# Optimization experiments

Hardware: AMD Instinct MI355X
Metric: run time of the kernel (lower is better)

## Reference

```python
import jax, jax.numpy as jnp
import numpy as np

N_NODES = 100000


def gcn_conv(x, edge_index, W, b):
    # PyG GCNConv: linear first, then symmetric-normalized aggregation with self-loops, then bias.
    n = x.shape[0]
    h = x @ W  # [N, out]
    loop = jnp.arange(n, dtype=edge_index.dtype)
    src = jnp.concatenate([edge_index[0], loop])  # source nodes (x_j)
    dst = jnp.concatenate([edge_index[1], loop])  # target nodes (aggregation index)
    ones = jnp.ones(dst.shape[0], dtype=h.dtype)
    deg = jax.ops.segment_sum(ones, dst, num_segments=n)  # in-degree incl. self-loop
    dinv = jnp.where(deg > 0, jax.lax.rsqrt(deg), 0.0)
    norm = dinv[src] * dinv[dst]  # [E+N]
    msgs = h[src] * norm[:, None]  # gather + scale
    out = jax.ops.segment_sum(msgs, dst, num_segments=n)  # scatter-add
    return out + b


def setup_inputs() -> dict:
    key = jax.random.key(0)
    k1, k2, k3, k4 = jax.random.split(key, 4)
    x = jax.random.normal(k1, (N_NODES, 128), dtype=jnp.float32)
    edge_index = jax.random.randint(k2, (2, 3200000), 0, N_NODES, dtype=jnp.int64)
    W1 = jax.random.normal(k3, (128, 16), dtype=jnp.float32) * (1.0 / np.sqrt(128))
    b1 = jnp.zeros((16,), dtype=jnp.float32)
    W2 = jax.random.normal(k4, (16, 10), dtype=jnp.float32) * (1.0 / np.sqrt(16))
    b2 = jnp.zeros((10,), dtype=jnp.float32)
    return {"x": x, "edge_index": edge_index, "W1": W1, "b1": b1, "W2": W2, "b2": b2}


def reference(x, edge_index, W1, b1, W2, b2):
    h = gcn_conv(x, edge_index, W1, b1)
    h = jax.nn.relu(h)
    h = gcn_conv(h, edge_index, W2, b2)
    return jax.nn.log_softmax(h, axis=1)
```

## Files before the change

### kernel.cpp

```cpp
#include <hip/hip_runtime.h>
#include <hip/hip_fp16.h>
#include <math.h>

#define NN 100000
#define F0 128
#define F1 16
#define F2 10
#define NBUCK 391
#define TILE 8192
#define EPT 16
#define CAP 16384
#define BPT 512

__device__ inline void fma4(float4& a, float s, const float4& w) {
  a.x = fmaf(s, w.x, a.x);
  a.y = fmaf(s, w.y, a.y);
  a.z = fmaf(s, w.z, a.z);
  a.w = fmaf(s, w.w, a.w);
}

__device__ inline unsigned pk2(float a, float b) {
  __half ha = __float2half(a), hb = __float2half(b);
  return (unsigned)__half_as_ushort(ha) | ((unsigned)__half_as_ushort(hb) << 16);
}

__device__ inline float2 up2(unsigned u) {
  __half2 h;
  *(unsigned*)&h = u;
  return __half22float2(h);
}

__device__ inline void nt_store_f2(float a, float b, float* p) {
  union { double d; float f[2]; } u;
  u.f[0] = a; u.f[1] = b;
  __builtin_nontemporal_store(u.d, (double*)p);
}

__global__ void k_zero(int* __restrict__ bucket_cnt) {
  int i = blockIdx.x * blockDim.x + threadIdx.x;
  if (i < NBUCK) bucket_cnt[i] = 0;
}

__global__ __launch_bounds__(256) void k_bincount(const int* __restrict__ dst, int E,
                                                  int* __restrict__ bucket_cnt) {
  __shared__ int hist[NBUCK];
  int t = threadIdx.x;
  for (int i = t; i < NBUCK; i += 256) hist[i] = 0;
  __syncthreads();
  int per = (E + gridDim.x - 1) / gridDim.x;
  int e0 = blockIdx.x * per, e1 = min(E, e0 + per);
  for (int e = e0 + t; e < e1; e += 256)
    atomicAdd(&hist[__builtin_nontemporal_load(dst + e) >> 8], 1);
  __syncthreads();
  for (int i = t; i < NBUCK; i += 256)
    if (hist[i]) atomicAdd(&bucket_cnt[i], hist[i]);
}

__global__ void k_binscan(const int* __restrict__ bucket_cnt, int* __restrict__ bucket_base,
                          int* __restrict__ bucket_cur) {
  __shared__ int lds[512];
  int t = threadIdx.x;
  int v = (t < NBUCK) ? bucket_cnt[t] : 0;
  lds[t] = v;
  __syncthreads();
  for (int o = 1; o < 512; o <<= 1) {
    int add = (t >= o) ? lds[t - o] : 0;
    __syncthreads();
    lds[t] += add;
    __syncthreads();
  }
  if (t < NBUCK) {
    int excl = lds[t] - v;
    bucket_base[t] = excl;
    bucket_cur[t] = excl;
    if (t == NBUCK - 1) bucket_base[NBUCK] = lds[t];
  }
}

__global__ __launch_bounds__(BPT) void k_binplace(const int* __restrict__ src,
                                                  const int* __restrict__ dst, int E,
                                                  int* __restrict__ bucket_cur,
                                                  int* __restrict__ packed) {
  __shared__ int cnt[NBUCK];
  __shared__ int loff[NBUCK];
  __shared__ int gbase[NBUCK];
  __shared__ int part[256];
  __shared__ int stage[TILE];
  int t = threadIdx.x;
  int e0 = blockIdx.x * TILE, e1 = min(E, e0 + TILE);
  int total = e1 - e0;
  for (int i = t; i < NBUCK; i += BPT) cnt[i] = 0;
  __syncthreads();
  int bkpos[EPT];
  int pval[EPT];
#pragma unroll
  for (int k = 0; k < EPT; k++) {
    int e = e0 + t + k * BPT;
    if (e < e1) {
      int d = __builtin_nontemporal_load(dst + e);
      int s = __builtin_nontemporal_load(src + e);
      int bk = d >> 8;
      int pos = atomicAdd(&cnt[bk], 1);
      bkpos[k] = (bk << 13) | pos;
      pval[k] = (s << 8) | (d & 255);
    } else {
      bkpos[k] = -1;
    }
  }
  __syncthreads();
  for (int i = t; i < NBUCK; i += BPT) {
    int c = cnt[i];
    gbase[i] = c ? atomicAdd(&bucket_cur[i], c) : 0;
  }
  if (t < 256) {
    int i0 = 2 * t, i1 = 2 * t + 1;
    int c0 = (i0 < NBUCK) ? cnt[i0] : 0;
    int c1 = (i1 < NBUCK) ? cnt[i1] : 0;
    part[t] = c0 + c1;
  }
  __syncthreads();
  for (int o = 1; o < 256; o <<= 1) {
    int add = 0;
    if (t < 256 && t >= o) add = part[t - o];
    __syncthreads();
    if (t < 256) part[t] += add;
    __syncthreads();
  }
  if (t < 256) {
    int i0 = 2 * t, i1 = 2 * t + 1;
    int c0 = (i0 < NBUCK) ? cnt[i0] : 0;
    int c1 = (i1 < NBUCK) ? cnt[i1] : 0;
    int excl = part[t] - c0 - c1;
    if (i0 < NBUCK) loff[i0] = excl;
    if (i1 < NBUCK) loff[i1] = excl + c0;
  }
  __syncthreads();
#pragma unroll
  for (int k = 0; k < EPT; k++) {
    if (bkpos[k] >= 0) {
      int bk = bkpos[k] >> 13, pos = bkpos[k] & 8191;
      stage[loff[bk] + pos] = pval[k];
    }
  }
  __syncthreads();
  int sub = t >> 4, lane = t & 15;
  for (int bk = sub; bk < NBUCK; bk += BPT / 16) {
    int lo = loff[bk];
    int hi = (bk + 1 < NBUCK) ? loff[bk + 1] : total;
    int gb = gbase[bk];
    for (int i = lo + lane; i < hi; i += 16) packed[gb + (i - lo)] = stage[i];
  }
}

__global__ __launch_bounds__(256) void k_bucket(const int* __restrict__ packed,
                                                const int* __restrict__ bucket_base,
                                                int* __restrict__ row_start,
                                                float* __restrict__ dinv,
                                                int* __restrict__ col, int E) {
  __shared__ int stage[CAP];
  __shared__ int hist[256];
  __shared__ int off[256];
  __shared__ int cur[256];
  int b = blockIdx.x, t = threadIdx.x;
  int base = bucket_base[b];
  int cnt = bucket_base[b + 1] - base;
  hist[t] = 0;
  bool staged = (cnt <= CAP);
  if (staged)
    for (int i = t; i < cnt; i += 256) stage[i] = __builtin_nontemporal_load(packed + base + i);
  __syncthreads();
  if (staged) {
    for (int i = t; i < cnt; i += 256) atomicAdd(&hist[stage[i] & 255], 1);
  } else {
    for (int i = t; i < cnt; i += 256) atomicAdd(&hist[packed[base + i] & 255], 1);
  }
  __syncthreads();
  int v = hist[t];
  off[t] = v;
  __syncthreads();
  for (int o = 1; o < 256; o <<= 1) {
    int add = (t >= o) ? off[t - o] : 0;
    __syncthreads();
    off[t] += add;
    __syncthreads();
  }
  int excl = off[t] - v;
  cur[t] = excl;
  int d = b * 256 + t;
  if (d < NN) {
    row_start[d] = base + excl;
    dinv[d] = rsqrtf((float)(v + 1));
  }
  if (b == 0 && t == 0) row_start[NN] = E;
  __syncthreads();
  if (staged) {
    for (int i = t; i < cnt; i += 256) {
      int p = stage[i];
      int pos = atomicAdd(&cur[p & 255], 1);
      col[base + pos] = p >> 8;
    }
  } else {
    for (int i = t; i < cnt; i += 256) {
      int p = packed[base + i];
      int pos = atomicAdd(&cur[p & 255], 1);
      col[base + pos] = p >> 8;
    }
  }
}

__global__ __launch_bounds__(256) void k_lin1(const float* __restrict__ x,
                                              const float* __restrict__ W1,
                                              const float* __restrict__ dinv,
                                              unsigned* __restrict__ tab1) {
  __shared__ float4 wl[F0 * 4];
  int t = threadIdx.x;
  for (int i = t; i < F0 * 4; i += 256) wl[i] = ((const float4*)W1)[i];
  __syncthreads();
  int row0 = (blockIdx.x * 256 + t) * 4;
  if (row0 >= NN) return;
  float4 acc[4][4];
#pragma unroll
  for (int r = 0; r < 4; r++)
#pragma unroll
    for (int j = 0; j < 4; j++) acc[r][j] = make_float4(0.f, 0.f, 0.f, 0.f);
  const float4* xr0 = (const float4*)(x + (size_t)(row0 + 0) * F0);
  const float4* xr1 = (const float4*)(x + (size_t)(row0 + 1) * F0);
  const float4* xr2 = (const float4*)(x + (size_t)(row0 + 2) * F0);
  const float4* xr3 = (const float4*)(x + (size_t)(row0 + 3) * F0);
  for (int k4 = 0; k4 < F0 / 4; k4++) {
    float4 xv[4];
    xv[0] = xr0[k4]; xv[1] = xr1[k4]; xv[2] = xr2[k4]; xv[3] = xr3[k4];
#pragma unroll
    for (int kk = 0; kk < 4; kk++) {
      float4 w0 = wl[(k4 * 4 + kk) * 4 + 0];
      float4 w1 = wl[(k4 * 4 + kk) * 4 + 1];
      float4 w2 = wl[(k4 * 4 + kk) * 4 + 2];
      float4 w3 = wl[(k4 * 4 + kk) * 4 + 3];
#pragma unroll
      for (int r = 0; r < 4; r++) {
        float xs = kk == 0 ? xv[r].x : kk == 1 ? xv[r].y : kk == 2 ? xv[r].z : xv[r].w;
        fma4(acc[r][0], xs, w0);
        fma4(acc[r][1], xs, w1);
        fma4(acc[r][2], xs, w2);
        fma4(acc[r][3], xs, w3);
      }
    }
  }
#pragma unroll
  for (int r = 0; r < 4; r++) {
    float dd = dinv[row0 + r];
    float4 a0 = acc[r][0], a1 = acc[r][1], a2 = acc[r][2], a3 = acc[r][3];
    uint4 o0, o1;
    o0.x = pk2(dd * a0.x, dd * a0.y);
    o0.y = pk2(dd * a0.z, dd * a0.w);
    o0.z = pk2(dd * a1.x, dd * a1.y);
    o0.w = pk2(dd * a1.z, dd * a1.w);
    o1.x = pk2(dd * a2.x, dd * a2.y);
    o1.y = pk2(dd * a2.z, dd * a2.w);
    o1.z = pk2(dd * a3.x, dd * a3.y);
    o1.w = pk2(dd * a3.z, dd * a3.w);
    uint4* orow = (uint4*)(tab1 + (size_t)(row0 + r) * 8);
    orow[0] = o0;
    orow[1] = o1;
  }
}

__global__ __launch_bounds__(256) void k_agg1(const uint4* __restrict__ tab1,
                                              const int* __restrict__ row_start,
                                              const int* __restrict__ col,
                                              const float* __restrict__ dinv,
                                              const float* __restrict__ b1,
                                              const float* __restrict__ W2g,
                                              unsigned* __restrict__ tab2) {
  __shared__ float w2[F1][F2];
  __shared__ float b1l[F1];
  int t = threadIdx.x;
  if (t < F1 * F2) w2[t / F2][t % F2] = W2g[t];
  if (t < F1) b1l[t] = b1[t];
  __syncthreads();
  int g = blockIdx.x * 256 + t;
  int d = g >> 2, q = g & 3;
  if (d >= NN) return;
  float a[16];
#pragma unroll
  for (int j = 0; j < 16; j++) a[j] = 0.f;
  auto addrow = [&](int s) {
    uint4 v0 = tab1[2 * s];
    uint4 v1 = tab1[2 * s + 1];
    float2 f;
    f = up2(v0.x); a[0] += f.x; a[1] += f.y;
    f = up2(v0.y); a[2] += f.x; a[3] += f.y;
    f = up2(v0.z); a[4] += f.x; a[5] += f.y;
    f = up2(v0.w); a[6] += f.x; a[7] += f.y;
    f = up2(v1.x); a[8] += f.x; a[9] += f.y;
    f = up2(v1.y); a[10] += f.x; a[11] += f.y;
    f = up2(v1.z); a[12] += f.x; a[13] += f.y;
    f = up2(v1.w); a[14] += f.x; a[15] += f.y;
  };
  if (q == 0) addrow(d);
  int e = row_start[d] + q, e1 = row_start[d + 1];
  for (; e + 4 < e1; e += 8) {
    int s0 = __builtin_nontemporal_load(col + e);
    int s1 = __builtin_nontemporal_load(col + e + 4);
    addrow(s0);
    addrow(s1);
  }
  if (e < e1) addrow(__builtin_nontemporal_load(col + e));
#pragma unroll
  for (int j = 0; j < 16; j++) a[j] += __shfl_xor(a[j], 1);
#pragma unroll
  for (int j = 0; j < 16; j++) a[j] += __shfl_xor(a[j], 2);
  if (q >= 2) return;
  float dd = dinv[d];
  float h[16];
#pragma unroll
  for (int j = 0; j < 16; j++) h[j] = fmaxf(fmaf(dd, a[j], b1l[j]), 0.f);
  if (q == 0) {
    float p[8];
#pragma unroll
    for (int j = 0; j < 8; j++) {
      float s = 0.f;
#pragma unroll
      for (int kk = 0; kk < 16; kk++) s = fmaf(h[kk], w2[kk][j], s);
      p[j] = s;
    }
    uint4 o;
    o.x = pk2(dd * p[0], dd * p[1]);
    o.y = pk2(dd * p[2], dd * p[3]);
    o.z = pk2(dd * p[4], dd * p[5]);
    o.w = pk2(dd * p[6], dd * p[7]);
    *(uint4*)(tab2 + (size_t)d * 8) = o;
  } else {
    float p8 = 0.f, p9 = 0.f;
#pragma unroll
    for (int kk = 0; kk < 16; kk++) {
      p8 = fmaf(h[kk], w2[kk][8], p8);
      p9 = fmaf(h[kk], w2[kk][9], p9);
    }
    tab2[(size_t)d * 8 + 4] = pk2(dd * p8, dd * p9);
  }
}

__global__ __launch_bounds__(256) void k_agg2(const unsigned* __restrict__ tab2,
                                              const int* __restrict__ row_start,
                                              const int* __restrict__ col,
                                              const float* __restrict__ dinv,
                                              const float* __restrict__ b2,
                                              float* __restrict__ out) {
  __shared__ float b2l[F2];
  int t = threadIdx.x;
  if (t < F2) b2l[t] = b2[t];
  __syncthreads();
  int g = blockIdx.x * 256 + t;
  int d = g >> 2, q = g & 3;
  if (d >= NN) return;
  float a[10];
#pragma unroll
  for (int j = 0; j < 10; j++) a[j] = 0.f;
  auto addrow = [&](int s) {
    uint4 v = *(const uint4*)(tab2 + (size_t)s * 8);
    unsigned w = tab2[(size_t)s * 8 + 4];
    float2 f;
    f = up2(v.x); a[0] += f.x; a[1] += f.y;
    f = up2(v.y); a[2] += f.x; a[3] += f.y;
    f = up2(v.z); a[4] += f.x; a[5] += f.y;
    f = up2(v.w); a[6] += f.x; a[7] += f.y;
    f = up2(w);   a[8] += f.x; a[9] += f.y;
  };
  if (q == 0) addrow(d);
  int e = row_start[d] + q, e1 = row_start[d + 1];
  for (; e + 4 < e1; e += 8) {
    int s0 = __builtin_nontemporal_load(col + e);
    int s1 = __builtin_nontemporal_load(col + e + 4);
    addrow(s0);
    addrow(s1);
  }
  if (e < e1) addrow(__builtin_nontemporal_load(col + e));
#pragma unroll
  for (int j = 0; j < 10; j++) a[j] += __shfl_xor(a[j], 1);
#pragma unroll
  for (int j = 0; j < 10; j++) a[j] += __shfl_xor(a[j], 2);
  if (q >= 3) return;
  float dd = dinv[d];
  float v[10];
#pragma unroll
  for (int j = 0; j < F2; j++) v[j] = fmaf(dd, a[j], b2l[j]);
  float m = v[0];
#pragma unroll
  for (int j = 1; j < F2; j++) m = fmaxf(m, v[j]);
  float sum = 0.f;
#pragma unroll
  for (int j = 0; j < F2; j++) sum += expf(v[j] - m);
  float lse = m + logf(sum);
  float* o = out + (size_t)d * F2;
  if (q == 0) {
    nt_store_f2(v[0] - lse, v[1] - lse, o + 0);
    nt_store_f2(v[2] - lse, v[3] - lse, o + 2);
  } else if (q == 1) {
    nt_store_f2(v[4] - lse, v[5] - lse, o + 4);
    nt_store_f2(v[6] - lse, v[7] - lse, o + 6);
  } else {
    nt_store_f2(v[8] - lse, v[9] - lse, o + 8);
  }
}

extern "C" void kernel_launch(void* const* d_in, const int* in_sizes, int n_in,
                              void* d_out, int out_size, void* d_ws, size_t ws_size,
                              hipStream_t stream) {
  const float* x  = (const float*)d_in[0];
  const int*   ei = (const int*)d_in[1];
  const float* W1 = (const float*)d_in[2];
  const float* b1 = (const float*)d_in[3];
  const float* W2 = (const float*)d_in[4];
  const float* b2 = (const float*)d_in[5];
  float* out = (float*)d_out;
  int E = in_sizes[1] / 2;
  const int* src = ei;
  const int* dst = ei + E;

  char* p = (char*)d_ws;
  auto alloc = [&](size_t bytes) {
    char* r = p;
    p += (bytes + 255) & ~(size_t)255;
    return r;
  };
  size_t tabsz = (size_t)NN * 8 * 4;
  float* dinv        = (float*)alloc((size_t)NN * 4);
  int*   row_start   = (int*)alloc((size_t)(NN + 1) * 4);
  int*   bucket_cnt  = (int*)alloc((size_t)NBUCK * 4);
  int*   bucket_base = (int*)alloc((size_t)(NBUCK + 1) * 4);
  int*   bucket_cur  = (int*)alloc((size_t)NBUCK * 4);
  int*   col         = (int*)alloc((size_t)E * 4);
  size_t needA = tabsz * 2;
  size_t regA = (size_t)E * 4;
  char*  A = (char*)alloc(regA > needA ? regA : needA);
  int*      packed = (int*)A;
  unsigned* tab1 = (unsigned*)A;
  unsigned* tab2 = (unsigned*)(A + tabsz);

  int nblk4N = (4 * NN + 255) / 256;
  int nblk_place = (E + TILE - 1) / TILE;
  hipLaunchKernelGGL(k_zero, dim3(2), dim3(256), 0, stream, bucket_cnt);
  hipLaunchKernelGGL(k_bincount, dim3(1024), dim3(256), 0, stream, dst, E, bucket_cnt);
  hipLaunchKernelGGL(k_binscan, dim3(1), dim3(512), 0, stream, bucket_cnt, bucket_base, bucket_cur);
  hipLaunchKernelGGL(k_binplace, dim3(nblk_place), dim3(BPT), 0, stream, src, dst, E, bucket_cur, packed);
  hipLaunchKernelGGL(k_bucket, dim3(NBUCK), dim3(256), 0, stream, packed, bucket_base, row_start, dinv, col, E);
  hipLaunchKernelGGL(k_lin1, dim3((NN / 4 + 255) / 256), dim3(256), 0, stream, x, W1, dinv, tab1);
  hipLaunchKernelGGL(k_agg1, dim3(nblk4N), dim3(256), 0, stream,
                     (const uint4*)tab1, row_start, col, dinv, b1, W2, tab2);
  hipLaunchKernelGGL(k_agg2, dim3(nblk4N), dim3(256), 0, stream, tab2, row_start, col, dinv, b2, out);
}
```

Measured before the change: 195.7 us.

## Split aggregation by feature columns across the four lanes of each node

```diff
diff --git a/kernel.cpp b/kernel.cpp
--- a/kernel.cpp
+++ b/kernel.cpp
@@ -265,7 +265,7 @@
   }
 }
 
-__global__ __launch_bounds__(256) void k_agg1(const uint4* __restrict__ tab1,
+__global__ __launch_bounds__(256) void k_agg1(const unsigned* __restrict__ tab1,
                                               const int* __restrict__ row_start,
                                               const int* __restrict__ col,
                                               const float* __restrict__ dinv,
@@ -281,64 +281,53 @@
   int g = blockIdx.x * 256 + t;
   int d = g >> 2, q = g & 3;
   if (d >= NN) return;
-  float a[16];
-#pragma unroll
-  for (int j = 0; j < 16; j++) a[j] = 0.f;
+  const uint2* T = (const uint2*)tab1;
+  float a0 = 0.f, a1 = 0.f, a2 = 0.f, a3 = 0.f;
   auto addrow = [&](int s) {
-    uint4 v0 = tab1[2 * s];
-    uint4 v1 = tab1[2 * s + 1];
-    float2 f;
-    f = up2(v0.x); a[0] += f.x; a[1] += f.y;
-    f = up2(v0.y); a[2] += f.x; a[3] += f.y;
-    f = up2(v0.z); a[4] += f.x; a[5] += f.y;
-    f = up2(v0.w); a[6] += f.x; a[7] += f.y;
-    f = up2(v1.x); a[8] += f.x; a[9] += f.y;
-    f = up2(v1.y); a[10] += f.x; a[11] += f.y;
-    f = up2(v1.z); a[12] += f.x; a[13] += f.y;
-    f = up2(v1.w); a[14] += f.x; a[15] += f.y;
+    uint2 v = T[(size_t)s * 4 + q];
+    float2 f0 = up2(v.x), f1 = up2(v.y);
+    a0 += f0.x; a1 += f0.y; a2 += f1.x; a3 += f1.y;
   };
-  if (q == 0) addrow(d);
-  int e = row_start[d] + q, e1 = row_start[d + 1];
-  for (; e + 4 < e1; e += 8) {
+  addrow(d);
+  int e = row_start[d], e1 = row_start[d + 1];
+  for (; e + 3 < e1; e += 4) {
     int s0 = __builtin_nontemporal_load(col + e);
-    int s1 = __builtin_nontemporal_load(col + e + 4);
-    addrow(s0);
-    addrow(s1);
-  }
-  if (e < e1) addrow(__builtin_nontemporal_load(col + e));
-#pragma unroll
-  for (int j = 0; j < 16; j++) a[j] += __shfl_xor(a[j], 1);
-#pragma unroll
-  for (int j = 0; j < 16; j++) a[j] += __shfl_xor(a[j], 2);
-  if (q >= 2) return;
+    int s1 = __builtin_nontemporal_load(col + e + 1);
+    int s2 = __builtin_nontemporal_load(col + e + 2);
+    int s3 = __builtin_nontemporal_load(col + e + 3);
+    addrow(s0); addrow(s1); addrow(s2); addrow(s3);
+  }
+  for (; e < e1; e++) addrow(__builtin_nontemporal_load(col + e));
   float dd = dinv[d];
-  float h[16];
-#pragma unroll
-  for (int j = 0; j < 16; j++) h[j] = fmaxf(fmaf(dd, a[j], b1l[j]), 0.f);
+  float h[4];
+  h[0] = fmaxf(fmaf(dd, a0, b1l[q * 4 + 0]), 0.f);
+  h[1] = fmaxf(fmaf(dd, a1, b1l[q * 4 + 1]), 0.f);
+  h[2] = fmaxf(fmaf(dd, a2, b1l[q * 4 + 2]), 0.f);
+  h[3] = fmaxf(fmaf(dd, a3, b1l[q * 4 + 3]), 0.f);
+  float p[F2];
+#pragma unroll
+  for (int j = 0; j < F2; j++) {
+    float s = 0.f;
+#pragma unroll
+    for (int kk = 0; kk < 4; kk++) s = fmaf(h[kk], w2[q * 4 + kk][j], s);
+    p[j] = s;
+  }
+#pragma unroll
+  for (int j = 0; j < F2; j++) p[j] += __shfl_xor(p[j], 1);
+#pragma unroll
+  for (int j = 0; j < F2; j++) p[j] += __shfl_xor(p[j], 2);
+  uint2* O = (uint2*)tab2;
+  uint2 o;
   if (q == 0) {
-    float p[8];
-#pragma unroll
-    for (int j = 0; j < 8; j++) {
-      float s = 0.f;
-#pragma unroll
-      for (int kk = 0; kk < 16; kk++) s = fmaf(h[kk], w2[kk][j], s);
-      p[j] = s;
-    }
-    uint4 o;
-    o.x = pk2(dd * p[0], dd * p[1]);
-    o.y = pk2(dd * p[2], dd * p[3]);
-    o.z = pk2(dd * p[4], dd * p[5]);
-    o.w = pk2(dd * p[6], dd * p[7]);
-    *(uint4*)(tab2 + (size_t)d * 8) = o;
+    o.x = pk2(dd * p[0], dd * p[1]); o.y = pk2(dd * p[2], dd * p[3]);
+  } else if (q == 1) {
+    o.x = pk2(dd * p[4], dd * p[5]); o.y = pk2(dd * p[6], dd * p[7]);
+  } else if (q == 2) {
+    o.x = pk2(dd * p[8], dd * p[9]); o.y = 0u;
   } else {
-    float p8 = 0.f, p9 = 0.f;
-#pragma unroll
-    for (int kk = 0; kk < 16; kk++) {
-      p8 = fmaf(h[kk], w2[kk][8], p8);
-      p9 = fmaf(h[kk], w2[kk][9], p9);
-    }
-    tab2[(size_t)d * 8 + 4] = pk2(dd * p8, dd * p9);
-  }
+    o.x = 0u; o.y = 0u;
+  }
+  O[(size_t)d * 4 + q] = o;
 }
 
 __global__ __launch_bounds__(256) void k_agg2(const unsigned* __restrict__ tab2,
@@ -347,60 +336,51 @@
                                               const float* __restrict__ dinv,
                                               const float* __restrict__ b2,
                                               float* __restrict__ out) {
-  __shared__ float b2l[F2];
-  int t = threadIdx.x;
-  if (t < F2) b2l[t] = b2[t];
+  __shared__ float b2l[F1];
+  int t = threadIdx.x;
+  if (t < F1) b2l[t] = (t < F2) ? b2[t] : -1e30f;
   __syncthreads();
   int g = blockIdx.x * 256 + t;
   int d = g >> 2, q = g & 3;
   if (d >= NN) return;
-  float a[10];
-#pragma unroll
-  for (int j = 0; j < 10; j++) a[j] = 0.f;
+  const uint2* T = (const uint2*)tab2;
+  float a0 = 0.f, a1 = 0.f, a2 = 0.f, a3 = 0.f;
   auto addrow = [&](int s) {
-    uint4 v = *(const uint4*)(tab2 + (size_t)s * 8);
-    unsigned w = tab2[(size_t)s * 8 + 4];
-    float2 f;
-    f = up2(v.x); a[0] += f.x; a[1] += f.y;
-    f = up2(v.y); a[2] += f.x; a[3] += f.y;
-    f = up2(v.z); a[4] += f.x; a[5] += f.y;
-    f = up2(v.w); a[6] += f.x; a[7] += f.y;
-    f = up2(w);   a[8] += f.x; a[9] += f.y;
+    uint2 v = T[(size_t)s * 4 + q];
+    float2 f0 = up2(v.x), f1 = up2(v.y);
+    a0 += f0.x; a1 += f0.y; a2 += f1.x; a3 += f1.y;
   };
-  if (q == 0) addrow(d);
-  int e = row_start[d] + q, e1 = row_start[d + 1];
-  for (; e + 4 < e1; e += 8) {
+  addrow(d);
+  int e = row_start[d], e1 = row_start[d + 1];
+  for (; e + 3 < e1; e += 4) {
     int s0 = __builtin_nontemporal_load(col + e);
-    int s1 = __builtin_nontemporal_load(col + e + 4);
-    addrow(s0);
-    addrow(s1);
-  }
-  if (e < e1) addrow(__builtin_nontemporal_load(col + e));
-#pragma unroll
-  for (int j = 0; j < 10; j++) a[j] += __shfl_xor(a[j], 1);
-#pragma unroll
-  for (int j = 0; j < 10; j++) a[j] += __shfl_xor(a[j], 2);
-  if (q >= 3) return;
+    int s1 = __builtin_nontemporal_load(col + e + 1);
+    int s2 = __builtin_nontemporal_load(col + e + 2);
+    int s3 = __builtin_nontemporal_load(col + e + 3);
+    addrow(s0); addrow(s1); addrow(s2); addrow(s3);
+  }
+  for (; e < e1; e++) addrow(__builtin_nontemporal_load(col + e));
   float dd = dinv[d];
-  float v[10];
-#pragma unroll
-  for (int j = 0; j < F2; j++) v[j] = fmaf(dd, a[j], b2l[j]);
-  float m = v[0];
-#pragma unroll
-  for (int j = 1; j < F2; j++) m = fmaxf(m, v[j]);
-  float sum = 0.f;
-#pragma unroll
-  for (int j = 0; j < F2; j++) sum += expf(v[j] - m);
+  float v0 = fmaf(dd, a0, b2l[q * 4 + 0]);
+  float v1 = fmaf(dd, a1, b2l[q * 4 + 1]);
+  float v2 = fmaf(dd, a2, b2l[q * 4 + 2]);
+  float v3 = fmaf(dd, a3, b2l[q * 4 + 3]);
+  float m = fmaxf(fmaxf(v0, v1), fmaxf(v2, v3));
+  m = fmaxf(m, __shfl_xor(m, 1));
+  m = fmaxf(m, __shfl_xor(m, 2));
+  float sum = expf(v0 - m) + expf(v1 - m) + expf(v2 - m) + expf(v3 - m);
+  sum += __shfl_xor(sum, 1);
+  sum += __shfl_xor(sum, 2);
   float lse = m + logf(sum);
   float* o = out + (size_t)d * F2;
   if (q == 0) {
-    nt_store_f2(v[0] - lse, v[1] - lse, o + 0);
-    nt_store_f2(v[2] - lse, v[3] - lse, o + 2);
+    nt_store_f2(v0 - lse, v1 - lse, o + 0);
+    nt_store_f2(v2 - lse, v3 - lse, o + 2);
   } else if (q == 1) {
-    nt_store_f2(v[4] - lse, v[5] - lse, o + 4);
-    nt_store_f2(v[6] - lse, v[7] - lse, o + 6);
-  } else {
-    nt_store_f2(v[8] - lse, v[9] - lse, o + 8);
+    nt_store_f2(v0 - lse, v1 - lse, o + 4);
+    nt_store_f2(v2 - lse, v3 - lse, o + 6);
+  } else if (q == 2) {
+    nt_store_f2(v0 - lse, v1 - lse, o + 8);
   }
 }
 
@@ -447,6 +427,6 @@
   hipLaunchKernelGGL(k_bucket, dim3(NBUCK), dim3(256), 0, stream, packed, bucket_base, row_start, dinv, col, E);
   hipLaunchKernelGGL(k_lin1, dim3((NN / 4 + 255) / 256), dim3(256), 0, stream, x, W1, dinv, tab1);
   hipLaunchKernelGGL(k_agg1, dim3(nblk4N), dim3(256), 0, stream,
-                     (const uint4*)tab1, row_start, col, dinv, b1, W2, tab2);
+                     tab1, row_start, col, dinv, b1, W2, tab2);
   hipLaunchKernelGGL(k_agg2, dim3(nblk4N), dim3(256), 0, stream, tab2, row_start, col, dinv, b2, out);
 }
```

After: 200.9 us. 2.6% more time.
